# Kernel optimization log

Measured on AMD Instinct MI355X. Metric: run time of the kernel, lower is better.

The kernel has to match this reference:

```python
import jax, jax.numpy as jnp
import numpy as np

KNN = 16
BN_EPS = 1e-5


def _swiglu(z, w1, w2, w3):
    # SwiGLU applied over the last dim: w2(silu(w1 z) * (w3 z))
    return (jax.nn.silu(z @ w1.T) * (z @ w3.T)) @ w2.T


def setup_inputs() -> dict:
    key = jax.random.key(0)
    ks = jax.random.split(key, 12)
    B, T, D = 1, 2048, 768
    H, N, KD = 4, 25600, 128
    HID_A, HID_S = 44, 1024
    inp = {
        "x": jax.random.normal(ks[0], (B, T, D), jnp.float32),
        "wq": jax.random.normal(ks[1], (H * KD, D), jnp.float32) * (1.0 / np.sqrt(D)),
        "bq": jax.random.normal(ks[2], (H * KD,), jnp.float32) * 0.02,
        "bn_gamma": jnp.ones((H * KD,), jnp.float32),
        "bn_beta": jnp.zeros((H * KD,), jnp.float32),
        "bn_mean": jnp.zeros((H * KD,), jnp.float32),
        "bn_var": jnp.ones((H * KD,), jnp.float32),
        "keys": jax.random.uniform(ks[3], (H, N, KD), jnp.float32, -1.0 / np.sqrt(KD), 1.0 / np.sqrt(KD)),
        "w_down_tab": jax.random.normal(ks[4], (N, 1), jnp.float32) * 0.02,
        "w_up_tab": jax.random.normal(ks[5], (N, 1), jnp.float32) * 0.02,
        "a_w1": jax.random.normal(ks[6], (HID_A, KNN), jnp.float32) * (1.0 / np.sqrt(KNN)),
        "a_w2": jax.random.normal(ks[7], (KNN, HID_A), jnp.float32) * (1.0 / np.sqrt(HID_A)),
        "a_w3": jax.random.normal(ks[8], (HID_A, KNN), jnp.float32) * (1.0 / np.sqrt(KNN)),
        "s_w1": jax.random.normal(ks[9], (HID_S, D), jnp.float32) * (1.0 / np.sqrt(D)),
        "s_w2": jax.random.normal(ks[10], (D, HID_S), jnp.float32) * (1.0 / np.sqrt(HID_S)),
        "s_w3": jax.random.normal(ks[11], (HID_S, D), jnp.float32) * (1.0 / np.sqrt(D)),
    }
    return inp


def reference(x, wq, bq, bn_gamma, bn_beta, bn_mean, bn_var, keys,
              w_down_tab, w_up_tab, a_w1, a_w2, a_w3, s_w1, s_w2, s_w3):
    B, T, D = x.shape
    H, N, KD = keys.shape
    identity = x
    # query projection + BatchNorm1d (inference: running stats)
    q = x.reshape(-1, D) @ wq.T + bq                      # (bs, H*KD)
    q = (q - bn_mean) * jax.lax.rsqrt(bn_var + BN_EPS) * bn_gamma + bn_beta
    q = q.reshape(-1, H, KD)                              # (bs, H, KD)
    # product-key scoring against full key table, per head
    scores = jnp.einsum('bhk,hnk->bhn', q, keys)          # (bs, H, N)
    top_s, top_i = jax.lax.top_k(scores, KNN)             # (bs, H, KNN)
    gates = jax.nn.softmax(top_s, axis=-1)
    idx = top_i.reshape(B, T, H, KNN)
    gates = gates.reshape(B, T, H, KNN)
    # expert_dim == 1: embedding gather yields a scalar per selected expert
    w_down = w_down_tab[idx, 0]                           # (B, T, H, KNN)
    w_up = w_up_tab[idx, 0]                               # (B, T, H, KNN)
    # einsum('btd,bthkd->bthk') with d-broadcast (expert_dim=1 vs D):
    # equals sum_d x[b,t,d] * w_down[b,t,h,k,0]
    xd = jnp.sum(x, axis=-1)[:, :, None, None] * w_down   # (B, T, H, KNN)
    h = _swiglu(xd, a_w1, a_w2, a_w3)                     # (B, T, H, KNN)
    h = h * gates
    # einsum('bthk,bthkd->btd') with d=1 -> (B, T, 1), broadcasts vs (B,T,D)
    comb = jnp.sum(h * w_up, axis=(2, 3))[:, :, None]     # (B, T, 1)
    out = comb + _swiglu(identity, s_w1, s_w2, s_w3)      # (B, T, D)
    return out
```

## Files before the change

kernel.cpp:

```cpp
#include <hip/hip_runtime.h>
#include <hip/hip_bf16.h>
#include <cmath>

#define NEG_INF (-3.402823466e38f)
#define SPLITS 32
#define SPN    800
#define GRP    32
#define NGRP   25

typedef __attribute__((ext_vector_type(8))) short s16x8;
typedef __attribute__((ext_vector_type(4))) float f32x4;

__device__ __forceinline__ unsigned short f2bf(float f) {
    union { float f; unsigned u; } v; v.f = f;
    unsigned u = v.u;
    u += 0x7fffu + ((u >> 16) & 1u);
    return (unsigned short)(u >> 16);
}

__global__ __launch_bounds__(256) void cvt_all_kernel(
        const float* __restrict__ s0, const float* __restrict__ s1,
        const float* __restrict__ s2, const float* __restrict__ s3,
        const float* __restrict__ s4, const float* __restrict__ keys,
        unsigned short* __restrict__ dst, float* __restrict__ sumx) {
    int i = blockIdx.x * 256 + threadIdx.x;
    if (i >= 4358144) return;
    const float* src; int base;
    if      (i < 393216)  { src = s0;   base = 0; }
    else if (i < 491520)  { src = s1;   base = 393216; }
    else if (i < 688128)  { src = s2;   base = 491520; }
    else if (i < 884736)  { src = s3;   base = 688128; }
    else if (i < 1081344) { src = s4;   base = 884736; }
    else                  { src = keys; base = 1081344; }
    float4 f = ((const float4*)src)[i - base];
    ushort4 o;
    o.x = f2bf(f.x); o.y = f2bf(f.y); o.z = f2bf(f.z); o.w = f2bf(f.w);
    ((ushort4*)dst)[i] = o;
    if (i < 393216) {
        float s = f.x + f.y + f.z + f.w;
        #pragma unroll
        for (int off = 32; off > 0; off >>= 1) s += __shfl_down(s, off);
        if ((threadIdx.x & 63) == 0) atomicAdd(&sumx[i / 192], s);
    }
}

template <int EPI>
__global__ __launch_bounds__(256) void gemm_nt(
        const unsigned short* __restrict__ A, const unsigned short* __restrict__ W,
        int M, int N, int K,
        float* __restrict__ outF, unsigned short* __restrict__ outB,
        const float* __restrict__ p0, const float* __restrict__ p1,
        const float* __restrict__ p2, const float* __restrict__ p3,
        const float* __restrict__ p4) {
    __shared__ alignas(16) short As[64][72];
    __shared__ alignas(16) short Ws[64][72];
    const int tid = threadIdx.x;
    const int m0 = blockIdx.x * 64, n0 = blockIdx.y * 64;
    const int wv = tid >> 6, lane = tid & 63;
    const int wr = wv >> 1, wc = wv & 1;
    const int lr = lane & 15, lq = lane >> 4;
    f32x4 acc[2][2];
    #pragma unroll
    for (int i = 0; i < 2; ++i)
        #pragma unroll
        for (int j = 0; j < 2; ++j) acc[i][j] = (f32x4){0.f, 0.f, 0.f, 0.f};

    for (int kb = 0; kb < K; kb += 64) {
        #pragma unroll
        for (int it = 0; it < 2; ++it) {
            int chunk = tid + it * 256;
            int row = chunk >> 3, c8 = (chunk & 7) * 8;
            *(s16x8*)&As[row][c8] = *(const s16x8*)(A + (size_t)(m0 + row) * K + kb + c8);
            *(s16x8*)&Ws[row][c8] = *(const s16x8*)(W + (size_t)(n0 + row) * K + kb + c8);
        }
        __syncthreads();
        #pragma unroll
        for (int ks = 0; ks < 2; ++ks) {
            const int k0 = ks * 32 + lq * 8;
            #pragma unroll
            for (int rt = 0; rt < 2; ++rt) {
                s16x8 a = *(const s16x8*)&As[wr * 32 + rt * 16 + lr][k0];
                #pragma unroll
                for (int ct = 0; ct < 2; ++ct) {
                    s16x8 b = *(const s16x8*)&Ws[wc * 32 + ct * 16 + lr][k0];
                    acc[rt][ct] = __builtin_amdgcn_mfma_f32_16x16x32_bf16(a, b, acc[rt][ct], 0, 0, 0);
                }
            }
        }
        __syncthreads();
    }
    #pragma unroll
    for (int rt = 0; rt < 2; ++rt)
        #pragma unroll
        for (int ct = 0; ct < 2; ++ct)
            #pragma unroll
            for (int r = 0; r < 4; ++r) {
                int m = m0 + wr * 32 + rt * 16 + lq * 4 + r;
                int n = n0 + wc * 32 + ct * 16 + lr;
                float v = acc[rt][ct][r];
                if (EPI == 0) {
                    float q = v + p0[n];
                    q = (q - p3[n]) * rsqrtf(p4[n] + 1e-5f) * p1[n] + p2[n];
                    outB[(size_t)m * N + n] = f2bf(q);
                } else {
                    outF[(size_t)m * N + n] = v + p0[m];
                }
            }
}

__device__ __forceinline__ void swiglu_body(
        int sb, int tid, const unsigned short* __restrict__ A,
        const unsigned short* __restrict__ W1, const unsigned short* __restrict__ W3,
        unsigned short* __restrict__ outB, char* smem) {
    short (*As)[72]  = (short(*)[72])smem;
    short (*W1s)[72] = (short(*)[72])(smem + 9216);
    short (*W3s)[72] = (short(*)[72])(smem + 18432);
    const int m0 = (sb & 31) * 64, n0 = (sb >> 5) * 64;
    const int wv = tid >> 6, lane = tid & 63;
    const int wr = wv >> 1, wc = wv & 1;
    const int lr = lane & 15, lq = lane >> 4;
    f32x4 acc1[2][2], acc3[2][2];
    #pragma unroll
    for (int i = 0; i < 2; ++i)
        #pragma unroll
        for (int j = 0; j < 2; ++j) {
            acc1[i][j] = (f32x4){0.f, 0.f, 0.f, 0.f};
            acc3[i][j] = (f32x4){0.f, 0.f, 0.f, 0.f};
        }
    for (int kb = 0; kb < 768; kb += 64) {
        #pragma unroll
        for (int it = 0; it < 2; ++it) {
            int chunk = tid + it * 256;
            int row = chunk >> 3, c8 = (chunk & 7) * 8;
            *(s16x8*)&As[row][c8]  = *(const s16x8*)(A  + (size_t)(m0 + row) * 768 + kb + c8);
            *(s16x8*)&W1s[row][c8] = *(const s16x8*)(W1 + (size_t)(n0 + row) * 768 + kb + c8);
            *(s16x8*)&W3s[row][c8] = *(const s16x8*)(W3 + (size_t)(n0 + row) * 768 + kb + c8);
        }
        __syncthreads();
        #pragma unroll
        for (int ks = 0; ks < 2; ++ks) {
            const int k0 = ks * 32 + lq * 8;
            #pragma unroll
            for (int rt = 0; rt < 2; ++rt) {
                s16x8 a = *(const s16x8*)&As[wr * 32 + rt * 16 + lr][k0];
                #pragma unroll
                for (int ct = 0; ct < 2; ++ct) {
                    s16x8 b1 = *(const s16x8*)&W1s[wc * 32 + ct * 16 + lr][k0];
                    s16x8 b3 = *(const s16x8*)&W3s[wc * 32 + ct * 16 + lr][k0];
                    acc1[rt][ct] = __builtin_amdgcn_mfma_f32_16x16x32_bf16(a, b1, acc1[rt][ct], 0, 0, 0);
                    acc3[rt][ct] = __builtin_amdgcn_mfma_f32_16x16x32_bf16(a, b3, acc3[rt][ct], 0, 0, 0);
                }
            }
        }
        __syncthreads();
    }
    #pragma unroll
    for (int rt = 0; rt < 2; ++rt)
        #pragma unroll
        for (int ct = 0; ct < 2; ++ct)
            #pragma unroll
            for (int r = 0; r < 4; ++r) {
                int m = m0 + wr * 32 + rt * 16 + lq * 4 + r;
                int n = n0 + wc * 32 + ct * 16 + lr;
                float u1 = acc1[rt][ct][r], u3 = acc3[rt][ct][r];
                float hv = u1 / (1.f + expf(-u1)) * u3;
                outB[(size_t)m * 1024 + n] = f2bf(hv);
            }
}

__device__ __forceinline__ void down_body(
        int sb, int tid, const unsigned short* __restrict__ A,
        const unsigned short* __restrict__ W, float* __restrict__ outF,
        char* smem) {
    short (*As)[72] = (short(*)[72])smem;
    short (*Ws)[72] = (short(*)[72])(smem + 9216);
    const int m0 = (sb & 31) * 64, n0 = (sb >> 5) * 64;
    const int wv = tid >> 6, lane = tid & 63;
    const int wr = wv >> 1, wc = wv & 1;
    const int lr = lane & 15, lq = lane >> 4;
    f32x4 acc[2][2];
    #pragma unroll
    for (int i = 0; i < 2; ++i)
        #pragma unroll
        for (int j = 0; j < 2; ++j) acc[i][j] = (f32x4){0.f, 0.f, 0.f, 0.f};
    for (int kb = 0; kb < 1024; kb += 64) {
        #pragma unroll
        for (int it = 0; it < 2; ++it) {
            int chunk = tid + it * 256;
            int row = chunk >> 3, c8 = (chunk & 7) * 8;
            *(s16x8*)&As[row][c8] = *(const s16x8*)(A + (size_t)(m0 + row) * 1024 + kb + c8);
            *(s16x8*)&Ws[row][c8] = *(const s16x8*)(W + (size_t)(n0 + row) * 1024 + kb + c8);
        }
        __syncthreads();
        #pragma unroll
        for (int ks = 0; ks < 2; ++ks) {
            const int k0 = ks * 32 + lq * 8;
            #pragma unroll
            for (int rt = 0; rt < 2; ++rt) {
                s16x8 a = *(const s16x8*)&As[wr * 32 + rt * 16 + lr][k0];
                #pragma unroll
                for (int ct = 0; ct < 2; ++ct) {
                    s16x8 b = *(const s16x8*)&Ws[wc * 32 + ct * 16 + lr][k0];
                    acc[rt][ct] = __builtin_amdgcn_mfma_f32_16x16x32_bf16(a, b, acc[rt][ct], 0, 0, 0);
                }
            }
        }
        __syncthreads();
    }
    #pragma unroll
    for (int rt = 0; rt < 2; ++rt)
        #pragma unroll
        for (int ct = 0; ct < 2; ++ct)
            #pragma unroll
            for (int r = 0; r < 4; ++r) {
                int m = m0 + wr * 32 + rt * 16 + lq * 4 + r;
                int n = n0 + wc * 32 + ct * 16 + lr;
                outF[(size_t)m * 768 + n] = acc[rt][ct][r];
            }
}

template <int PASS>
__device__ __forceinline__ void score_body(
        int b, int tid,
        const unsigned short* __restrict__ Q, const unsigned short* __restrict__ Kt,
        float* __restrict__ maxbuf, const float* __restrict__ theta,
        int* __restrict__ cnt, float2* __restrict__ buf, char* smem) {
    short (*Ks)[GRP][136] = (short(*)[GRP][136])smem;
    const int tile = b >> 7;
    const int hsp = b & 127;
    const int h = hsp >> 5, sp = hsp & 31;
    const int w = tid >> 6, lane = tid & 63;
    const int lr = lane & 15, lq = lane >> 4;
    const int t0 = tile * 256 + w * 64;
    const int nb0 = sp * SPN;

    s16x8 qf[4][4];
    #pragma unroll
    for (int tt = 0; tt < 4; ++tt) {
        const unsigned short* qp = Q + (size_t)(t0 + tt * 16 + lr) * 512 + h * 128 + lq * 8;
        #pragma unroll
        for (int ks = 0; ks < 4; ++ks) qf[tt][ks] = *(const s16x8*)(qp + ks * 32);
    }

    float runmax[4] = {NEG_INF, NEG_INF, NEG_INF, NEG_INF};
    float th[4];
    if (PASS == 2) {
        #pragma unroll
        for (int tt = 0; tt < 4; ++tt) th[tt] = theta[(t0 + tt * 16 + lr) * 4 + h];
    }

    const int srow = tid >> 4;
    const int scol = (tid & 15) * 8;
    const unsigned short* kgp =
        Kt + ((size_t)h * 25600 + nb0 + srow) * 128 + scol;

    {
        *(s16x8*)&Ks[0][srow][scol]      = *(const s16x8*)kgp;
        *(s16x8*)&Ks[0][srow + 16][scol] = *(const s16x8*)(kgp + 2048);
    }

    for (int g = 0; g < NGRP; ++g) {
        s16x8 ka0, ka1;
        if (g + 1 < NGRP) {
            const unsigned short* kp = kgp + (size_t)(g + 1) * 4096;
            ka0 = *(const s16x8*)kp;
            ka1 = *(const s16x8*)(kp + 2048);
        }
        __syncthreads();
        const int cb = g & 1;
        #pragma unroll
        for (int st = 0; st < 2; ++st) {
            f32x4 acc[4];
            #pragma unroll
            for (int tt = 0; tt < 4; ++tt) acc[tt] = (f32x4){0.f, 0.f, 0.f, 0.f};
            #pragma unroll
            for (int ks = 0; ks < 4; ++ks) {
                s16x8 ka = *(const s16x8*)&Ks[cb][st * 16 + lr][ks * 32 + lq * 8];
                #pragma unroll
                for (int tt = 0; tt < 4; ++tt)
                    acc[tt] = __builtin_amdgcn_mfma_f32_16x16x32_bf16(ka, qf[tt][ks], acc[tt], 0, 0, 0);
            }
            if (PASS == 1) {
                #pragma unroll
                for (int tt = 0; tt < 4; ++tt) {
                    float m0 = fmaxf(fmaxf(acc[tt][0], acc[tt][1]),
                                     fmaxf(acc[tt][2], acc[tt][3]));
                    runmax[tt] = fmaxf(runmax[tt], m0);
                }
            } else {
                const int nb = nb0 + g * GRP + st * 16;
                #pragma unroll
                for (int tt = 0; tt < 4; ++tt) {
                    float m0 = fmaxf(fmaxf(acc[tt][0], acc[tt][1]),
                                     fmaxf(acc[tt][2], acc[tt][3]));
                    if (m0 >= th[tt]) {
                        int g4 = (t0 + tt * 16 + lr) * 4 + h;
                        #pragma unroll
                        for (int r = 0; r < 4; ++r) {
                            if (acc[tt][r] >= th[tt]) {
                                int n = nb + lq * 4 + r;
                                int pos = atomicAdd(&cnt[g4], 1);
                                if (pos < 64) {
                                    float2 e; e.x = acc[tt][r]; e.y = __int_as_float(n);
                                    buf[(size_t)g4 * 64 + pos] = e;
                                }
                            }
                        }
                    }
                }
            }
        }
        if (g + 1 < NGRP) {
            const int nbuf = cb ^ 1;
            *(s16x8*)&Ks[nbuf][srow][scol]      = ka0;
            *(s16x8*)&Ks[nbuf][srow + 16][scol] = ka1;
        }
    }

    if (PASS == 1) {
        #pragma unroll
        for (int tt = 0; tt < 4; ++tt)
            maxbuf[(size_t)((t0 + tt * 16 + lr) * 4 + h) * 128 + sp * 4 + lq] = runmax[tt];
    }
}

template <int PASS>
__global__ __launch_bounds__(256, 4) void score_pass_kernel(
        const unsigned short* __restrict__ Q, const unsigned short* __restrict__ Kt,
        float* __restrict__ maxbuf, const float* __restrict__ theta,
        int* __restrict__ cnt, float2* __restrict__ buf) {
    __shared__ alignas(16) char smem[17408];
    score_body<PASS>(blockIdx.x, threadIdx.x, Q, Kt, maxbuf, theta, cnt, buf, smem);
}

__global__ __launch_bounds__(256, 4) void megaA_kernel(
        const unsigned short* __restrict__ xb, const unsigned short* __restrict__ w1,
        const unsigned short* __restrict__ w3, unsigned short* __restrict__ hb,
        const unsigned short* __restrict__ Q, const unsigned short* __restrict__ Kt,
        float* __restrict__ maxbuf) {
    __shared__ alignas(16) char smem[27648];
    if (blockIdx.x < 512)
        swiglu_body(blockIdx.x, threadIdx.x, xb, w1, w3, hb, smem);
    else
        score_body<1>(blockIdx.x - 512, threadIdx.x, Q, Kt, maxbuf,
                      nullptr, nullptr, nullptr, smem);
}

__global__ __launch_bounds__(256, 4) void megaB_kernel(
        const unsigned short* __restrict__ hb, const unsigned short* __restrict__ w2,
        float* __restrict__ outF,
        const unsigned short* __restrict__ Q, const unsigned short* __restrict__ Kt,
        const float* __restrict__ theta, int* __restrict__ cnt,
        float2* __restrict__ buf) {
    __shared__ alignas(16) char smem[18432];
    if (blockIdx.x < 384)
        down_body(blockIdx.x, threadIdx.x, hb, w2, outF, smem);
    else
        score_body<2>(blockIdx.x - 384, threadIdx.x, Q, Kt, nullptr,
                      theta, cnt, buf, smem);
}

__global__ __launch_bounds__(64) void theta_kernel(
        const float* __restrict__ maxbuf, float* __restrict__ theta) {
    int g = blockIdx.x * 64 + threadIdx.x;
    if (g >= 8192) return;
    const float* mb = maxbuf + (size_t)g * 128;
    float s[16];
    #pragma unroll
    for (int i = 0; i < 16; ++i) s[i] = NEG_INF;
    for (int j = 0; j < 128; ++j) {
        float v = mb[j];
        if (v > s[15]) {
            #pragma unroll
            for (int i = 15; i > 0; --i)
                s[i] = (v > s[i - 1]) ? s[i - 1] : ((v > s[i]) ? v : s[i]);
            s[0] = (v > s[0]) ? v : s[0];
        }
    }
    theta[g] = s[15];
}

template <int FUSE_OUT>
__global__ __launch_bounds__(256) void finalize_kernel(
        const int* __restrict__ cnt, const float2* __restrict__ buf,
        const float* __restrict__ sumx,
        const float* __restrict__ wdown, const float* __restrict__ wup,
        const float* __restrict__ aw1, const float* __restrict__ aw2,
        const float* __restrict__ aw3, float* __restrict__ combsum,
        float* __restrict__ out) {
    __shared__ float zsh[4][16];
    __shared__ float wsh[4][16];
    __shared__ float csh[4];
    const int wv = threadIdx.x >> 6, lane = threadIdx.x & 63;
    const int t = blockIdx.x;
    const int g = t * 4 + wv;
    int c = cnt[g]; c = (c > 64) ? 64 : c;

    float v = NEG_INF; int n = 0x7fffffff;
    if (lane < c) {
        float2 e = buf[(size_t)g * 64 + lane];
        v = e.x; n = __float_as_int(e.y);
    }
    int r = 0;
    for (int i = 0; i < c; ++i) {
        float vi = __shfl(v, i);
        int   ni = __shfl(n, i);
        r += ((vi > v) || (vi == v && ni < n)) ? 1 : 0;
    }
    float m = v;
    #pragma unroll
    for (int off = 32; off > 0; off >>= 1) m = fmaxf(m, __shfl_xor(m, off));
    const bool sel = (lane < c) && (r < 16);
    float e = sel ? expf(v - m) : 0.f;
    float den = e;
    #pragma unroll
    for (int off = 32; off > 0; off >>= 1) den += __shfl_xor(den, off);
    if (sel) {
        zsh[wv][r] = sumx[t] * wdown[n];
        wsh[wv][r] = (e / den) * wup[n];
    }
    __syncthreads();
    float contrib = 0.f;
    if (lane < 44) {
        float u1 = 0.f, u3 = 0.f, cj = 0.f;
        #pragma unroll
        for (int k = 0; k < 16; ++k) {
            float zk = zsh[wv][k];
            u1 += zk * aw1[lane * 16 + k];
            u3 += zk * aw3[lane * 16 + k];
            cj += wsh[wv][k] * aw2[k * 44 + lane];
        }
        float gj = u1 / (1.f + expf(-u1)) * u3;
        contrib = gj * cj;
    }
    #pragma unroll
    for (int off = 32; off > 0; off >>= 1) contrib += __shfl_xor(contrib, off);
    if (FUSE_OUT) {
        if (lane == 0) csh[wv] = contrib;
        __syncthreads();
        float comb = csh[0] + csh[1] + csh[2] + csh[3];
        float* orow = out + (size_t)t * 768;
        #pragma unroll
        for (int i = 0; i < 3; ++i) orow[threadIdx.x + i * 256] += comb;
    } else {
        if (lane == 0) atomicAdd(&combsum[t], contrib);
    }
}

__global__ __launch_bounds__(256) void gemm_swiglu_kernel(
        const unsigned short* __restrict__ A, const unsigned short* __restrict__ W1,
        const unsigned short* __restrict__ W3, unsigned short* __restrict__ outB) {
    __shared__ alignas(16) char smem[27648];
    swiglu_body(blockIdx.x, threadIdx.x, A, W1, W3, outB, smem);
}

extern "C" void kernel_launch(void* const* d_in, const int* in_sizes, int n_in,
                              void* d_out, int out_size, void* d_ws, size_t ws_size,
                              hipStream_t stream) {
    const float* x     = (const float*)d_in[0];
    const float* wq    = (const float*)d_in[1];
    const float* bq    = (const float*)d_in[2];
    const float* gamma = (const float*)d_in[3];
    const float* beta  = (const float*)d_in[4];
    const float* mean  = (const float*)d_in[5];
    const float* var   = (const float*)d_in[6];
    const float* keys  = (const float*)d_in[7];
    const float* wdown = (const float*)d_in[8];
    const float* wup   = (const float*)d_in[9];
    const float* aw1   = (const float*)d_in[10];
    const float* aw2   = (const float*)d_in[11];
    const float* aw3   = (const float*)d_in[12];
    const float* sw1   = (const float*)d_in[13];
    const float* sw2   = (const float*)d_in[14];
    const float* sw3   = (const float*)d_in[15];
    float* out = (float*)d_out;

    char* ws = (char*)d_ws;
    unsigned short* x_b    = (unsigned short*)(ws + 0);
    unsigned short* wq_b   = (unsigned short*)(ws + 3145728);
    unsigned short* sw1_b  = (unsigned short*)(ws + 3932160);
    unsigned short* sw3_b  = (unsigned short*)(ws + 5505024);
    unsigned short* sw2_b  = (unsigned short*)(ws + 7077888);
    unsigned short* keys_b = (unsigned short*)(ws + 8650752);
    unsigned short* q_b    = (unsigned short*)(ws + 34865152);
    float* sumx    = (float*)(ws + 36962304);
    float* theta   = (float*)(ws + 36970496);
    float* combsum = (float*)(ws + 37003264);
    int*   cnt     = (int*)  (ws + 37011456);
    char* R1 = ws + 37044224;
    float* maxbuf = (float*)R1;
    float2* buf   = (float2*)R1;
    unsigned short* h_b_fused = (unsigned short*)(ws + 41238528);
    const bool fused = ws_size >= 45432832ull;

    hipMemsetAsync(ws + 36962304, 0, 81920, stream);
    cvt_all_kernel<<<17024, 256, 0, stream>>>(x, wq, sw1, sw3, sw2, keys, x_b, sumx);
    gemm_nt<0><<<dim3(32, 8), 256, 0, stream>>>(x_b, wq_b, 2048, 512, 768,
                                                nullptr, q_b, bq, gamma, beta, mean, var);
    if (fused) {
        megaA_kernel<<<1536, 256, 0, stream>>>(x_b, sw1_b, sw3_b, h_b_fused,
                                               q_b, keys_b, maxbuf);
        theta_kernel<<<128, 64, 0, stream>>>(maxbuf, theta);
        megaB_kernel<<<1408, 256, 0, stream>>>(h_b_fused, sw2_b, out,
                                               q_b, keys_b, theta, cnt, buf);
        finalize_kernel<1><<<2048, 256, 0, stream>>>(cnt, buf, sumx, wdown, wup,
                                                     aw1, aw2, aw3, combsum, out);
    } else {
        unsigned short* h_b = (unsigned short*)R1;
        score_pass_kernel<1><<<1024, 256, 0, stream>>>(q_b, keys_b, maxbuf, nullptr, nullptr, nullptr);
        theta_kernel<<<128, 64, 0, stream>>>(maxbuf, theta);
        score_pass_kernel<2><<<1024, 256, 0, stream>>>(q_b, keys_b, nullptr, theta, cnt, buf);
        finalize_kernel<0><<<2048, 256, 0, stream>>>(cnt, buf, sumx, wdown, wup,
                                                     aw1, aw2, aw3, combsum, nullptr);
        gemm_swiglu_kernel<<<512, 256, 0, stream>>>(x_b, sw1_b, sw3_b, h_b);
        gemm_nt<2><<<dim3(32, 12), 256, 0, stream>>>(h_b, sw2_b, 2048, 768, 1024,
                                                     out, nullptr, combsum,
                                                     nullptr, nullptr, nullptr, nullptr);
    }
}
```

Before: 313.9 us.

## Load key fragments directly from global memory in score pass, drop LDS staging

The scoring loop no longer stages key tiles through double-buffered shared memory with __syncthreads. Each wave now reads its 16-key MFMA fragments straight from global memory every sub-step. This removes LDS writes, reads and block barriers. The cost is that the four waves in a block each fetch the same keys redundantly, relying on L1/L2, and there is no explicit prefetch to hide load latency.

```diff
diff --git a/kernel.cpp b/kernel.cpp
--- a/kernel.cpp
+++ b/kernel.cpp
@@ -5,8 +5,7 @@
 #define NEG_INF (-3.402823466e38f)
 #define SPLITS 32
 #define SPN    800
-#define GRP    32
-#define NGRP   25
+#define NSUB   50
 
 typedef __attribute__((ext_vector_type(8))) short s16x8;
 typedef __attribute__((ext_vector_type(4))) float f32x4;
@@ -224,8 +223,7 @@
         int b, int tid,
         const unsigned short* __restrict__ Q, const unsigned short* __restrict__ Kt,
         float* __restrict__ maxbuf, const float* __restrict__ theta,
-        int* __restrict__ cnt, float2* __restrict__ buf, char* smem) {
-    short (*Ks)[GRP][136] = (short(*)[GRP][136])smem;
+        int* __restrict__ cnt, float2* __restrict__ buf) {
     const int tile = b >> 7;
     const int hsp = b & 127;
     const int h = hsp >> 5, sp = hsp & 31;
@@ -249,71 +247,60 @@
         for (int tt = 0; tt < 4; ++tt) th[tt] = theta[(t0 + tt * 16 + lr) * 4 + h];
     }
 
-    const int srow = tid >> 4;
-    const int scol = (tid & 15) * 8;
-    const unsigned short* kgp =
-        Kt + ((size_t)h * 25600 + nb0 + srow) * 128 + scol;
-
-    {
-        *(s16x8*)&Ks[0][srow][scol]      = *(const s16x8*)kgp;
-        *(s16x8*)&Ks[0][srow + 16][scol] = *(const s16x8*)(kgp + 2048);
-    }
-
-    for (int g = 0; g < NGRP; ++g) {
-        s16x8 ka0, ka1;
-        if (g + 1 < NGRP) {
-            const unsigned short* kp = kgp + (size_t)(g + 1) * 4096;
-            ka0 = *(const s16x8*)kp;
-            ka1 = *(const s16x8*)(kp + 2048);
-        }
-        __syncthreads();
-        const int cb = g & 1;
-        #pragma unroll
-        for (int st = 0; st < 2; ++st) {
-            f32x4 acc[4];
-            #pragma unroll
-            for (int tt = 0; tt < 4; ++tt) acc[tt] = (f32x4){0.f, 0.f, 0.f, 0.f};
-            #pragma unroll
-            for (int ks = 0; ks < 4; ++ks) {
-                s16x8 ka = *(const s16x8*)&Ks[cb][st * 16 + lr][ks * 32 + lq * 8];
-                #pragma unroll
-                for (int tt = 0; tt < 4; ++tt)
-                    acc[tt] = __builtin_amdgcn_mfma_f32_16x16x32_bf16(ka, qf[tt][ks], acc[tt], 0, 0, 0);
-            }
-            if (PASS == 1) {
-                #pragma unroll
-                for (int tt = 0; tt < 4; ++tt) {
-                    float m0 = fmaxf(fmaxf(acc[tt][0], acc[tt][1]),
-                                     fmaxf(acc[tt][2], acc[tt][3]));
-                    runmax[tt] = fmaxf(runmax[tt], m0);
-                }
-            } else {
-                const int nb = nb0 + g * GRP + st * 16;
-                #pragma unroll
-                for (int tt = 0; tt < 4; ++tt) {
-                    float m0 = fmaxf(fmaxf(acc[tt][0], acc[tt][1]),
-                                     fmaxf(acc[tt][2], acc[tt][3]));
-                    if (m0 >= th[tt]) {
-                        int g4 = (t0 + tt * 16 + lr) * 4 + h;
-                        #pragma unroll
-                        for (int r = 0; r < 4; ++r) {
-                            if (acc[tt][r] >= th[tt]) {
-                                int n = nb + lq * 4 + r;
-                                int pos = atomicAdd(&cnt[g4], 1);
-                                if (pos < 64) {
-                                    float2 e; e.x = acc[tt][r]; e.y = __int_as_float(n);
-                                    buf[(size_t)g4 * 64 + pos] = e;
-                                }
+    const unsigned short* kp0 =
+        Kt + ((size_t)h * 25600 + nb0 + lr) * 128 + lq * 8;
+
+    #pragma unroll 1
+    for (int s = 0; s < NSUB; ++s) {
+        const unsigned short* kp = kp0 + (size_t)s * 16 * 128;
+        s16x8 ka0 = *(const s16x8*)(kp);
+        s16x8 ka1 = *(const s16x8*)(kp + 32);
+        s16x8 ka2 = *(const s16x8*)(kp + 64);
+        s16x8 ka3 = *(const s16x8*)(kp + 96);
+        f32x4 acc[4];
+        #pragma unroll
+        for (int tt = 0; tt < 4; ++tt) acc[tt] = (f32x4){0.f, 0.f, 0.f, 0.f};
+        #pragma unroll
+        for (int tt = 0; tt < 4; ++tt)
+            acc[tt] = __builtin_amdgcn_mfma_f32_16x16x32_bf16(ka0, qf[tt][0], acc[tt], 0, 0, 0);
+        #pragma unroll
+        for (int tt = 0; tt < 4; ++tt)
+            acc[tt] = __builtin_amdgcn_mfma_f32_16x16x32_bf16(ka1, qf[tt][1], acc[tt], 0, 0, 0);
+        #pragma unroll
+        for (int tt = 0; tt < 4; ++tt)
+            acc[tt] = __builtin_amdgcn_mfma_f32_16x16x32_bf16(ka2, qf[tt][2], acc[tt], 0, 0, 0);
+        #pragma unroll
+        for (int tt = 0; tt < 4; ++tt)
+            acc[tt] = __builtin_amdgcn_mfma_f32_16x16x32_bf16(ka3, qf[tt][3], acc[tt], 0, 0, 0);
+
+        if (PASS == 1) {
+            #pragma unroll
+            for (int tt = 0; tt < 4; ++tt) {
+                float m0 = fmaxf(fmaxf(acc[tt][0], acc[tt][1]),
+                                 fmaxf(acc[tt][2], acc[tt][3]));
+                runmax[tt] = fmaxf(runmax[tt], m0);
+            }
+        } else {
+            const int nb = nb0 + s * 16;
+            #pragma unroll
+            for (int tt = 0; tt < 4; ++tt) {
+                float m0 = fmaxf(fmaxf(acc[tt][0], acc[tt][1]),
+                                 fmaxf(acc[tt][2], acc[tt][3]));
+                if (m0 >= th[tt]) {
+                    int g4 = (t0 + tt * 16 + lr) * 4 + h;
+                    #pragma unroll
+                    for (int r = 0; r < 4; ++r) {
+                        if (acc[tt][r] >= th[tt]) {
+                            int n = nb + lq * 4 + r;
+                            int pos = atomicAdd(&cnt[g4], 1);
+                            if (pos < 64) {
+                                float2 e; e.x = acc[tt][r]; e.y = __int_as_float(n);
+                                buf[(size_t)g4 * 64 + pos] = e;
                             }
                         }
                     }
                 }
             }
-        }
-        if (g + 1 < NGRP) {
-            const int nbuf = cb ^ 1;
-            *(s16x8*)&Ks[nbuf][srow][scol]      = ka0;
-            *(s16x8*)&Ks[nbuf][srow + 16][scol] = ka1;
         }
     }
 
@@ -329,8 +316,7 @@
         const unsigned short* __restrict__ Q, const unsigned short* __restrict__ Kt,
         float* __restrict__ maxbuf, const float* __restrict__ theta,
         int* __restrict__ cnt, float2* __restrict__ buf) {
-    __shared__ alignas(16) char smem[17408];
-    score_body<PASS>(blockIdx.x, threadIdx.x, Q, Kt, maxbuf, theta, cnt, buf, smem);
+    score_body<PASS>(blockIdx.x, threadIdx.x, Q, Kt, maxbuf, theta, cnt, buf);
 }
 
 __global__ __launch_bounds__(256, 4) void megaA_kernel(
@@ -343,7 +329,7 @@
         swiglu_body(blockIdx.x, threadIdx.x, xb, w1, w3, hb, smem);
     else
         score_body<1>(blockIdx.x - 512, threadIdx.x, Q, Kt, maxbuf,
-                      nullptr, nullptr, nullptr, smem);
+                      nullptr, nullptr, nullptr);
 }
 
 __global__ __launch_bounds__(256, 4) void megaB_kernel(
@@ -357,7 +343,7 @@
         down_body(blockIdx.x, threadIdx.x, hb, w2, outF, smem);
     else
         score_body<2>(blockIdx.x - 384, threadIdx.x, Q, Kt, nullptr,
-                      theta, cnt, buf, smem);
+                      theta, cnt, buf);
 }
 
 __global__ __launch_bounds__(64) void theta_kernel(
```

After: 407.7 us. 1.3x slower.
